# Kernel tuning notes

Hardware: AMD Instinct MI355X
Metric: run time of the kernel (lower is better)

Reference implementation:

```python
import jax, jax.numpy as jnp
import numpy as np

N = 20000      # nodes
E = 320000     # edges
D = 512        # width
L = 4          # layers
VOCAB = 256
MAX_POS = 256
EPS = 1e-5


def setup_inputs() -> dict:
    key = jax.random.key(0)
    ks = jax.random.split(key, 12)
    tokens = jax.random.randint(ks[0], (N,), 0, VOCAB)
    pos = jax.random.randint(ks[1], (N,), 0, MAX_POS)
    edge_index = jax.random.randint(ks[2], (2, E), 0, N)
    vocab_emb = jax.random.normal(ks[3], (VOCAB, D), jnp.float32) * 0.05
    pos_emb = jax.random.normal(ks[4], (MAX_POS, D), jnp.float32) * 0.05
    bn_gamma = jnp.ones((L, D), jnp.float32)
    bn_beta = jnp.zeros((L, D), jnp.float32)
    bn_mean = jax.random.normal(ks[5], (L, D), jnp.float32) * 0.1
    bn_var = jax.random.uniform(ks[6], (L, D), jnp.float32, 0.5, 1.5)
    W_rel = jax.random.normal(ks[7], (L, D, D), jnp.float32) * (1.0 / np.sqrt(D))
    b_rel = jnp.zeros((L, D), jnp.float32)
    W_root = jax.random.normal(ks[8], (L, D, D), jnp.float32) * (1.0 / np.sqrt(D))
    return {
        "tokens": tokens, "pos": pos, "edge_index": edge_index,
        "vocab_emb": vocab_emb, "pos_emb": pos_emb,
        "bn_gamma": bn_gamma, "bn_beta": bn_beta,
        "bn_mean": bn_mean, "bn_var": bn_var,
        "W_rel": W_rel, "b_rel": b_rel, "W_root": W_root,
    }


def reference(tokens, pos, edge_index, vocab_emb, pos_emb,
              bn_gamma, bn_beta, bn_mean, bn_var, W_rel, b_rel, W_root):
    src, dst = edge_index[0], edge_index[1]
    # in-degree for mean aggregation (clamped to 1 like PyG mean aggr)
    deg = jax.ops.segment_sum(jnp.ones((E,), jnp.float32), dst, num_segments=N)
    deg = jnp.maximum(deg, 1.0)[:, None]                     # [N,1]

    x = vocab_emb[tokens] + pos_emb[pos]                     # [N,D]
    for l in range(L):
        # BatchNorm1d, eval mode with running stats
        inv = bn_gamma[l] * jax.lax.rsqrt(bn_var[l] + EPS)
        x = (x - bn_mean[l]) * inv + bn_beta[l]
        # GraphConv: W_root x_i + W_rel * mean_{j->i} x_j + b
        agg = jax.ops.segment_sum(x[src], dst, num_segments=N) / deg
        x = agg @ W_rel[l].T + b_rel[l] + x @ W_root[l].T
        x = jax.nn.relu(x)
    return x
```

## Files before the change

kernel.cpp:

```cpp
#include <hip/hip_runtime.h>
#include <cstdint>

#define EPS 1e-5f

typedef __attribute__((ext_vector_type(8))) short bf16x8;
typedef __attribute__((ext_vector_type(4))) float f32x4;

__device__ __forceinline__ unsigned short f2bf(float x) {
    uint32_t u = __float_as_uint(x);
    u += 0x7fffu + ((u >> 16) & 1u);
    return (unsigned short)(u >> 16);
}
__device__ __forceinline__ uint32_t pack2(float lo, float hi) {
    return (uint32_t)f2bf(lo) | ((uint32_t)f2bf(hi) << 16);
}
__device__ __forceinline__ float bflo(uint32_t p) { return __uint_as_float(p << 16); }
__device__ __forceinline__ float bfhi(uint32_t p) { return __uint_as_float(p & 0xffff0000u); }

__device__ __forceinline__ void async_ld16(const void* g, const void* l) {
    __builtin_amdgcn_global_load_lds(
        (const __attribute__((address_space(1))) uint32_t*)(uintptr_t)g,
        (__attribute__((address_space(3))) uint32_t*)(uint32_t)(uintptr_t)l,
        16, 0, 0);
}

__global__ __launch_bounds__(256) void zero_kernel(int* __restrict__ p, int n) {
    int i = blockIdx.x * 256 + threadIdx.x;
    if (i < n) p[i] = 0;
}

__global__ __launch_bounds__(256) void count_kernel(const int* __restrict__ ei,
                                                    int* __restrict__ deg, int E) {
    int e = blockIdx.x * 256 + threadIdx.x;
    if (e < E) atomicAdd(&deg[ei[E + e]], 1);
}

__global__ __launch_bounds__(1024) void scan_kernel(const int* __restrict__ deg,
                                                    int* __restrict__ offsets,
                                                    int* __restrict__ cursor,
                                                    float* __restrict__ deginv, int N) {
    __shared__ int part[1024];
    const int t = threadIdx.x;
    const int CH = (N + 1023) >> 10;
    const int base = t * CH;
    int s = 0;
    for (int j = 0; j < CH; ++j) {
        int idx = base + j;
        if (idx < N) s += deg[idx];
    }
    part[t] = s;
    __syncthreads();
    for (int off = 1; off < 1024; off <<= 1) {
        int add = (t >= off) ? part[t - off] : 0;
        __syncthreads();
        part[t] += add;
        __syncthreads();
    }
    int run = (t == 0) ? 0 : part[t - 1];
    for (int j = 0; j < CH; ++j) {
        int idx = base + j;
        if (idx < N) {
            offsets[idx] = run;
            cursor[idx]  = run;
            int dgi = deg[idx];
            deginv[idx] = 1.0f / (float)(dgi > 0 ? dgi : 1);
            run += dgi;
        }
    }
    if (t == 1023) offsets[N] = run;
}

__global__ __launch_bounds__(256) void fill_kernel(const int* __restrict__ ei,
                                                   int* __restrict__ cursor,
                                                   int* __restrict__ csr, int E) {
    int e = blockIdx.x * 256 + threadIdx.x;
    if (e < E) {
        int dd = ei[E + e];
        int slot = atomicAdd(&cursor[dd], 1);
        csr[slot] = ei[e];
    }
}

__global__ __launch_bounds__(256) void embed_bn_kernel(const int* __restrict__ tok,
                                                       const int* __restrict__ pos,
                                                       const float* __restrict__ vemb,
                                                       const float* __restrict__ pemb,
                                                       const float* __restrict__ gamma,
                                                       const float* __restrict__ beta,
                                                       const float* __restrict__ mean,
                                                       const float* __restrict__ var,
                                                       uint32_t* __restrict__ Acat, int N) {
    const int idx = blockIdx.x * 256 + threadIdx.x;
    if (idx >= N * 128) return;
    const int row = idx >> 7;
    const int c = (idx & 127) * 4;
    const int tk = tok[row];
    const int ps = pos[row];
    const float4 a = *(const float4*)&vemb[(size_t)tk * 512 + c];
    const float4 b = *(const float4*)&pemb[(size_t)ps * 512 + c];
    const float4 g = *(const float4*)&gamma[c];
    const float4 be = *(const float4*)&beta[c];
    const float4 mn = *(const float4*)&mean[c];
    const float4 vr = *(const float4*)&var[c];
    const float y0 = (a.x + b.x - mn.x) * (g.x * rsqrtf(vr.x + EPS)) + be.x;
    const float y1 = (a.y + b.y - mn.y) * (g.y * rsqrtf(vr.y + EPS)) + be.y;
    const float y2 = (a.z + b.z - mn.z) * (g.z * rsqrtf(vr.z + EPS)) + be.z;
    const float y3 = (a.w + b.w - mn.w) * (g.w * rsqrtf(vr.w + EPS)) + be.w;
    uint2 o;
    o.x = pack2(y0, y1);
    o.y = pack2(y2, y3);
    *(uint2*)&Acat[(size_t)row * 512 + (c >> 1)] = o;
}

__global__ __launch_bounds__(256) void castW_kernel(const float* __restrict__ Wroot,
                                                    const float* __restrict__ Wrel,
                                                    uint32_t* __restrict__ Wcat) {
    const int p = blockIdx.x * 256 + threadIdx.x;
    const int o  = p >> 9;
    const int dp = p & 511;
    float2 v;
    if (dp < 256) v = *(const float2*)&Wroot[(size_t)o * 512 + dp * 2];
    else          v = *(const float2*)&Wrel[(size_t)o * 512 + (dp - 256) * 2];
    Wcat[(size_t)o * 512 + dp] = pack2(v.x, v.y);
}

__global__ __launch_bounds__(256) void aggregate_kernel(uint32_t* __restrict__ Acat,
                                                        const int* __restrict__ offsets,
                                                        const int* __restrict__ csr,
                                                        const float* __restrict__ deginv,
                                                        int N) {
    const int node = blockIdx.x * 4 + (threadIdx.x >> 6);
    if (node >= N) return;
    const int lane = threadIdx.x & 63;
    const int col = lane * 4;
    const int beg = offsets[node];
    const int end = offsets[node + 1];
    float s[8] = {0.f, 0.f, 0.f, 0.f, 0.f, 0.f, 0.f, 0.f};
    int e = beg;
    for (; e + 8 <= end; e += 8) {
        uint4 p[8];
#pragma unroll
        for (int j = 0; j < 8; ++j) {
            const int ij = csr[e + j];
            p[j] = *(const uint4*)&Acat[(size_t)ij * 512 + col];
        }
#pragma unroll
        for (int j = 0; j < 8; ++j) {
            s[0] += bflo(p[j].x); s[1] += bfhi(p[j].x);
            s[2] += bflo(p[j].y); s[3] += bfhi(p[j].y);
            s[4] += bflo(p[j].z); s[5] += bfhi(p[j].z);
            s[6] += bflo(p[j].w); s[7] += bfhi(p[j].w);
        }
    }
    for (; e < end; ++e) {
        const int i0 = csr[e];
        const uint4 p0 = *(const uint4*)&Acat[(size_t)i0 * 512 + col];
        s[0] += bflo(p0.x); s[1] += bfhi(p0.x);
        s[2] += bflo(p0.y); s[3] += bfhi(p0.y);
        s[4] += bflo(p0.z); s[5] += bfhi(p0.z);
        s[6] += bflo(p0.w); s[7] += bfhi(p0.w);
    }
    const float inv = deginv[node];
    uint4 o;
    o.x = pack2(s[0] * inv, s[1] * inv);
    o.y = pack2(s[2] * inv, s[3] * inv);
    o.z = pack2(s[4] * inv, s[5] * inv);
    o.w = pack2(s[6] * inv, s[7] * inv);
    *(uint4*)&Acat[(size_t)node * 512 + 256 + col] = o;
}

__global__ __launch_bounds__(256) void gemm_bt_bias_relu(const unsigned short* __restrict__ A,
                                                         const unsigned short* __restrict__ B,
                                                         const float* __restrict__ bias,
                                                         const float* __restrict__ gamma,
                                                         const float* __restrict__ beta,
                                                         const float* __restrict__ mean,
                                                         const float* __restrict__ var,
                                                         int last,
                                                         float* __restrict__ C,
                                                         unsigned short* __restrict__ Abn,
                                                         int M) {
    __shared__ __align__(16) unsigned short As[64 * 32];
    __shared__ __align__(16) unsigned short Bs[256 * 32];

    const int t    = threadIdx.x;
    const int lane = t & 63;
    const int wave = t >> 6;
    const int wn = wave * 64;
    const int bm = blockIdx.y;
    const int bn = blockIdx.x;

    const int r  = t >> 2;
    const int kc = t & 3;
    int ar = bm * 64 + r; if (ar >= M) ar = M - 1;
    const int br = bn * 256 + r;

    const unsigned short* ga  = A + (size_t)ar * 1024 + kc * 8;
    const unsigned short* gb0 = B + (size_t)br * 1024 + kc * 8;

    unsigned short* la  = &As[r * 32 + kc * 8];
    unsigned short* lb0 = &Bs[r * 32 + kc * 8];

    const f32x4 zero = {0.f, 0.f, 0.f, 0.f};
    f32x4 acc[4][4];
#pragma unroll
    for (int i = 0; i < 4; ++i)
#pragma unroll
        for (int j = 0; j < 4; ++j) acc[i][j] = zero;

    const int lm = lane & 15;
    const int q  = lane >> 4;

    for (int k0 = 0; k0 < 1024; k0 += 32) {
        async_ld16(ga + k0, la);
#pragma unroll
        for (int j = 0; j < 4; ++j)
            async_ld16(gb0 + (size_t)j * 64 * 1024 + k0, lb0 + j * 64 * 32);
        __syncthreads();

        bf16x8 afr[4], bfr[4];
#pragma unroll
        for (int mt = 0; mt < 4; ++mt)
            afr[mt] = *(const bf16x8*)&As[(mt * 16 + lm) * 32 + q * 8];
#pragma unroll
        for (int nt = 0; nt < 4; ++nt)
            bfr[nt] = *(const bf16x8*)&Bs[(wn + nt * 16 + lm) * 32 + q * 8];
#pragma unroll
        for (int mt = 0; mt < 4; ++mt)
#pragma unroll
            for (int nt = 0; nt < 4; ++nt)
                acc[mt][nt] = __builtin_amdgcn_mfma_f32_16x16x32_bf16(afr[mt], bfr[nt],
                                                                     acc[mt][nt], 0, 0, 0);
        __syncthreads();
    }

#pragma unroll
    for (int nt = 0; nt < 4; ++nt) {
        const int col = bn * 256 + wn + nt * 16 + lm;
        const float bv = bias[col];
        float bn_inv = 0.f, bn_mb = 0.f;
        if (!last) {
            bn_inv = gamma[col] * rsqrtf(var[col] + EPS);
            bn_mb  = mean[col];
        }
        const float bn_beta = last ? 0.f : beta[col];
#pragma unroll
        for (int mt = 0; mt < 4; ++mt) {
            const int row0 = bm * 64 + mt * 16 + q * 4;
#pragma unroll
            for (int i = 0; i < 4; ++i) {
                const int row = row0 + i;
                if (row < M) {
                    float v = acc[mt][nt][i] + bv;
                    v = v > 0.f ? v : 0.f;
                    if (last) {
                        C[(size_t)row * 512 + col] = v;
                    } else {
                        const float y = (v - bn_mb) * bn_inv + bn_beta;
                        Abn[(size_t)row * 1024 + col] = f2bf(y);
                    }
                }
            }
        }
    }
}

extern "C" void kernel_launch(void* const* d_in, const int* in_sizes, int n_in,
                              void* d_out, int out_size, void* d_ws, size_t ws_size,
                              hipStream_t stream) {
    const int*   tokens = (const int*)d_in[0];
    const int*   posi   = (const int*)d_in[1];
    const int*   ei     = (const int*)d_in[2];
    const float* vemb   = (const float*)d_in[3];
    const float* pemb   = (const float*)d_in[4];
    const float* gamma  = (const float*)d_in[5];
    const float* beta   = (const float*)d_in[6];
    const float* mean   = (const float*)d_in[7];
    const float* var    = (const float*)d_in[8];
    const float* Wrel   = (const float*)d_in[9];
    const float* brel   = (const float*)d_in[10];
    const float* Wroot  = (const float*)d_in[11];

    const int N = in_sizes[0];
    const int E = in_sizes[2] / 2;
    float* out = (float*)d_out;

    char* w = (char*)d_ws;
    int*      deg     = (int*)(w);
    int*      offsets = (int*)(w + 80000);
    int*      cursor  = (int*)(w + 160016);
    float*    deginv  = (float*)(w + 240032);
    int*      csr     = (int*)(w + 320048);
    uint32_t* Acat    = (uint32_t*)(w + 1600064);
    uint32_t* Wcat    = (uint32_t*)(w + 42560064);

    zero_kernel<<<(N + 255) / 256, 256, 0, stream>>>(deg, N);
    count_kernel<<<(E + 255) / 256, 256, 0, stream>>>(ei, deg, E);
    scan_kernel<<<1, 1024, 0, stream>>>(deg, offsets, cursor, deginv, N);
    fill_kernel<<<(E + 255) / 256, 256, 0, stream>>>(ei, cursor, csr, E);

    embed_bn_kernel<<<(N * 128 + 255) / 256, 256, 0, stream>>>(
        tokens, posi, vemb, pemb, gamma, beta, mean, var, Acat, N);

    for (int l = 0; l < 4; ++l) {
        const int last = (l == 3);
        castW_kernel<<<1024, 256, 0, stream>>>(Wroot + (size_t)l * 262144,
                                               Wrel + (size_t)l * 262144, Wcat);
        aggregate_kernel<<<(N + 3) / 4, 256, 0, stream>>>(Acat, offsets, csr, deginv, N);
        gemm_bt_bias_relu<<<dim3(2, (N + 63) / 64), 256, 0, stream>>>(
            (const unsigned short*)Acat, (const unsigned short*)Wcat, brel + l * 512,
            gamma + (l + 1) * 512, beta + (l + 1) * 512,
            mean + (l + 1) * 512, var + (l + 1) * 512,
            last, out, (unsigned short*)Acat, N);
    }
}
```

Before: 574.0 us.

## Feed MFMA straight from global into registers and split node/aggregate buffers

```diff
diff --git a/kernel.cpp b/kernel.cpp
--- a/kernel.cpp
+++ b/kernel.cpp
@@ -16,13 +16,6 @@
 }
 __device__ __forceinline__ float bflo(uint32_t p) { return __uint_as_float(p << 16); }
 __device__ __forceinline__ float bfhi(uint32_t p) { return __uint_as_float(p & 0xffff0000u); }
-
-__device__ __forceinline__ void async_ld16(const void* g, const void* l) {
-    __builtin_amdgcn_global_load_lds(
-        (const __attribute__((address_space(1))) uint32_t*)(uintptr_t)g,
-        (__attribute__((address_space(3))) uint32_t*)(uint32_t)(uintptr_t)l,
-        16, 0, 0);
-}
 
 __global__ __launch_bounds__(256) void zero_kernel(int* __restrict__ p, int n) {
     int i = blockIdx.x * 256 + threadIdx.x;
@@ -89,7 +82,7 @@
                                                        const float* __restrict__ beta,
                                                        const float* __restrict__ mean,
                                                        const float* __restrict__ var,
-                                                       uint32_t* __restrict__ Acat, int N) {
+                                                       uint32_t* __restrict__ X, int N) {
     const int idx = blockIdx.x * 256 + threadIdx.x;
     if (idx >= N * 128) return;
     const int row = idx >> 7;
@@ -109,7 +102,7 @@
     uint2 o;
     o.x = pack2(y0, y1);
     o.y = pack2(y2, y3);
-    *(uint2*)&Acat[(size_t)row * 512 + (c >> 1)] = o;
+    *(uint2*)&X[(size_t)row * 256 + (c >> 1)] = o;
 }
 
 __global__ __launch_bounds__(256) void castW_kernel(const float* __restrict__ Wroot,
@@ -124,7 +117,8 @@
     Wcat[(size_t)o * 512 + dp] = pack2(v.x, v.y);
 }
 
-__global__ __launch_bounds__(256) void aggregate_kernel(uint32_t* __restrict__ Acat,
+__global__ __launch_bounds__(256) void aggregate_kernel(const uint32_t* __restrict__ X,
+                                                        uint32_t* __restrict__ G,
                                                         const int* __restrict__ offsets,
                                                         const int* __restrict__ csr,
                                                         const float* __restrict__ deginv,
@@ -142,7 +136,7 @@
 #pragma unroll
         for (int j = 0; j < 8; ++j) {
             const int ij = csr[e + j];
-            p[j] = *(const uint4*)&Acat[(size_t)ij * 512 + col];
+            p[j] = *(const uint4*)&X[(size_t)ij * 256 + col];
         }
 #pragma unroll
         for (int j = 0; j < 8; ++j) {
@@ -154,7 +148,7 @@
     }
     for (; e < end; ++e) {
         const int i0 = csr[e];
-        const uint4 p0 = *(const uint4*)&Acat[(size_t)i0 * 512 + col];
+        const uint4 p0 = *(const uint4*)&X[(size_t)i0 * 256 + col];
         s[0] += bflo(p0.x); s[1] += bfhi(p0.x);
         s[2] += bflo(p0.y); s[3] += bfhi(p0.y);
         s[4] += bflo(p0.z); s[5] += bfhi(p0.z);
@@ -166,40 +160,40 @@
     o.y = pack2(s[2] * inv, s[3] * inv);
     o.z = pack2(s[4] * inv, s[5] * inv);
     o.w = pack2(s[6] * inv, s[7] * inv);
-    *(uint4*)&Acat[(size_t)node * 512 + 256 + col] = o;
-}
-
-__global__ __launch_bounds__(256) void gemm_bt_bias_relu(const unsigned short* __restrict__ A,
-                                                         const unsigned short* __restrict__ B,
-                                                         const float* __restrict__ bias,
-                                                         const float* __restrict__ gamma,
-                                                         const float* __restrict__ beta,
-                                                         const float* __restrict__ mean,
-                                                         const float* __restrict__ var,
-                                                         int last,
-                                                         float* __restrict__ C,
-                                                         unsigned short* __restrict__ Abn,
-                                                         int M) {
-    __shared__ __align__(16) unsigned short As[64 * 32];
-    __shared__ __align__(16) unsigned short Bs[256 * 32];
-
+    *(uint4*)&G[(size_t)node * 256 + col] = o;
+}
+
+__global__ __launch_bounds__(256) void gemm_reg_bias_relu(const unsigned short* __restrict__ X,
+                                                          const unsigned short* __restrict__ G,
+                                                          const unsigned short* __restrict__ B,
+                                                          const float* __restrict__ bias,
+                                                          const float* __restrict__ gamma,
+                                                          const float* __restrict__ beta,
+                                                          const float* __restrict__ mean,
+                                                          const float* __restrict__ var,
+                                                          int last,
+                                                          float* __restrict__ C,
+                                                          unsigned short* __restrict__ Y,
+                                                          int M) {
     const int t    = threadIdx.x;
     const int lane = t & 63;
     const int wave = t >> 6;
-    const int wn = wave * 64;
+    const int lm = lane & 15;
+    const int q  = lane >> 4;
     const int bm = blockIdx.y;
     const int bn = blockIdx.x;
-
-    const int r  = t >> 2;
-    const int kc = t & 3;
-    int ar = bm * 64 + r; if (ar >= M) ar = M - 1;
-    const int br = bn * 256 + r;
-
-    const unsigned short* ga  = A + (size_t)ar * 1024 + kc * 8;
-    const unsigned short* gb0 = B + (size_t)br * 1024 + kc * 8;
-
-    unsigned short* la  = &As[r * 32 + kc * 8];
-    unsigned short* lb0 = &Bs[r * 32 + kc * 8];
+    const int wn = bn * 256 + wave * 64;
+
+    uint32_t aoff[4], boff[4];
+#pragma unroll
+    for (int mt = 0; mt < 4; ++mt) {
+        int r = bm * 64 + mt * 16 + lm;
+        if (r >= M) r = M - 1;
+        aoff[mt] = (uint32_t)r * 512u + q * 8u;
+    }
+#pragma unroll
+    for (int nt = 0; nt < 4; ++nt)
+        boff[nt] = (uint32_t)(wn + nt * 16 + lm) * 1024u + q * 8u;
 
     const f32x4 zero = {0.f, 0.f, 0.f, 0.f};
     f32x4 acc[4][4];
@@ -208,42 +202,41 @@
 #pragma unroll
         for (int j = 0; j < 4; ++j) acc[i][j] = zero;
 
-    const int lm = lane & 15;
-    const int q  = lane >> 4;
-
-    for (int k0 = 0; k0 < 1024; k0 += 32) {
-        async_ld16(ga + k0, la);
-#pragma unroll
-        for (int j = 0; j < 4; ++j)
-            async_ld16(gb0 + (size_t)j * 64 * 1024 + k0, lb0 + j * 64 * 32);
-        __syncthreads();
-
-        bf16x8 afr[4], bfr[4];
-#pragma unroll
-        for (int mt = 0; mt < 4; ++mt)
-            afr[mt] = *(const bf16x8*)&As[(mt * 16 + lm) * 32 + q * 8];
-#pragma unroll
-        for (int nt = 0; nt < 4; ++nt)
-            bfr[nt] = *(const bf16x8*)&Bs[(wn + nt * 16 + lm) * 32 + q * 8];
-#pragma unroll
-        for (int mt = 0; mt < 4; ++mt)
-#pragma unroll
-            for (int nt = 0; nt < 4; ++nt)
-                acc[mt][nt] = __builtin_amdgcn_mfma_f32_16x16x32_bf16(afr[mt], bfr[nt],
-                                                                     acc[mt][nt], 0, 0, 0);
-        __syncthreads();
+#define LOADA(P, av, K0) { _Pragma("unroll") for (int i_ = 0; i_ < 4; ++i_) \
+        av[i_] = *(const bf16x8*)((P) + aoff[i_] + (K0)); }
+#define LOADB(bv, K0) { _Pragma("unroll") for (int i_ = 0; i_ < 4; ++i_) \
+        bv[i_] = *(const bf16x8*)(B + boff[i_] + (K0)); }
+#define MFMA16(av, bv) { _Pragma("unroll") for (int mt_ = 0; mt_ < 4; ++mt_) \
+        _Pragma("unroll") for (int nt_ = 0; nt_ < 4; ++nt_) \
+            acc[mt_][nt_] = __builtin_amdgcn_mfma_f32_16x16x32_bf16(av[mt_], bv[nt_], acc[mt_][nt_], 0, 0, 0); }
+
+#pragma unroll
+    for (int ph = 0; ph < 2; ++ph) {
+        const unsigned short* P = ph ? G : X;
+        const int kb = ph * 512;
+        bf16x8 a0[4], b0[4], a1[4], b1[4];
+        LOADA(P, a0, 0); LOADB(b0, kb);
+        for (int k0 = 0; k0 < 448; k0 += 64) {
+            LOADA(P, a1, k0 + 32); LOADB(b1, kb + k0 + 32);
+            MFMA16(a0, b0);
+            LOADA(P, a0, k0 + 64); LOADB(b0, kb + k0 + 64);
+            MFMA16(a1, b1);
+        }
+        LOADA(P, a1, 480); LOADB(b1, kb + 480);
+        MFMA16(a0, b0);
+        MFMA16(a1, b1);
     }
 
 #pragma unroll
     for (int nt = 0; nt < 4; ++nt) {
-        const int col = bn * 256 + wn + nt * 16 + lm;
+        const int col = wn + nt * 16 + lm;
         const float bv = bias[col];
-        float bn_inv = 0.f, bn_mb = 0.f;
+        float bn_inv = 0.f, bn_mb = 0.f, bn_beta = 0.f;
         if (!last) {
             bn_inv = gamma[col] * rsqrtf(var[col] + EPS);
             bn_mb  = mean[col];
-        }
-        const float bn_beta = last ? 0.f : beta[col];
+            bn_beta = beta[col];
+        }
 #pragma unroll
         for (int mt = 0; mt < 4; ++mt) {
             const int row0 = bm * 64 + mt * 16 + q * 4;
@@ -257,12 +250,15 @@
                         C[(size_t)row * 512 + col] = v;
                     } else {
                         const float y = (v - bn_mb) * bn_inv + bn_beta;
-                        Abn[(size_t)row * 1024 + col] = f2bf(y);
+                        Y[(size_t)row * 512 + col] = f2bf(y);
                     }
                 }
             }
         }
     }
+#undef LOADA
+#undef LOADB
+#undef MFMA16
 }
 
 extern "C" void kernel_launch(void* const* d_in, const int* in_sizes, int n_in,
@@ -291,8 +287,11 @@
     int*      cursor  = (int*)(w + 160016);
     float*    deginv  = (float*)(w + 240032);
     int*      csr     = (int*)(w + 320048);
-    uint32_t* Acat    = (uint32_t*)(w + 1600064);
+    uint32_t* X0      = (uint32_t*)(w + 1600064);
+    uint32_t* G       = (uint32_t*)(w + 22080064);
     uint32_t* Wcat    = (uint32_t*)(w + 42560064);
+    uint32_t* X1      = (uint32_t*)(w + 43608640);
+    const bool big = ws_size >= (size_t)43608640 + 20480000;
 
     zero_kernel<<<(N + 255) / 256, 256, 0, stream>>>(deg, N);
     count_kernel<<<(E + 255) / 256, 256, 0, stream>>>(ei, deg, E);
@@ -300,17 +299,21 @@
     fill_kernel<<<(E + 255) / 256, 256, 0, stream>>>(ei, cursor, csr, E);
 
     embed_bn_kernel<<<(N * 128 + 255) / 256, 256, 0, stream>>>(
-        tokens, posi, vemb, pemb, gamma, beta, mean, var, Acat, N);
-
+        tokens, posi, vemb, pemb, gamma, beta, mean, var, X0, N);
+
+    uint32_t* X = X0;
+    uint32_t* Y = big ? X1 : X0;
     for (int l = 0; l < 4; ++l) {
         const int last = (l == 3);
         castW_kernel<<<1024, 256, 0, stream>>>(Wroot + (size_t)l * 262144,
                                                Wrel + (size_t)l * 262144, Wcat);
-        aggregate_kernel<<<(N + 3) / 4, 256, 0, stream>>>(Acat, offsets, csr, deginv, N);
-        gemm_bt_bias_relu<<<dim3(2, (N + 63) / 64), 256, 0, stream>>>(
-            (const unsigned short*)Acat, (const unsigned short*)Wcat, brel + l * 512,
+        aggregate_kernel<<<(N + 3) / 4, 256, 0, stream>>>(X, G, offsets, csr, deginv, N);
+        gemm_reg_bias_relu<<<dim3(2, (N + 63) / 64), 256, 0, stream>>>(
+            (const unsigned short*)X, (const unsigned short*)G,
+            (const unsigned short*)Wcat, brel + l * 512,
             gamma + (l + 1) * 512, beta + (l + 1) * 512,
             mean + (l + 1) * 512, var + (l + 1) * 512,
-            last, out, (unsigned short*)Acat, N);
-    }
-}
+            last, out, (unsigned short*)Y, N);
+        uint32_t* tmp = X; X = Y; Y = tmp;
+    }
+}
```

Result: slower. 810.1 us (+41.1%).
